# Optimization experiments

Hardware: AMD Instinct MI355X
Metric: run time of the kernel (lower is better)

The kernel has to match this reference:

```python
import jax, jax.numpy as jnp
import numpy as np

D_MODEL, N_HEADS, HEAD_DIM = 384, 12, 32
N_QP, N_VP = 4, 8
B, L = 2, 1024
OUT_DIM = N_HEADS * (HEAD_DIM + N_VP * 3 + N_VP)  # 12*(32+24+8)=768
LN_EPS = 1e-5


def _linear_params(key, din, dout):
    kw, _ = jax.random.split(key)
    W = jax.random.normal(kw, (din, dout), dtype=jnp.float32) / np.sqrt(din).astype(np.float32)
    b = jnp.zeros((dout,), dtype=jnp.float32)
    return W, b


def setup_inputs() -> dict:
    key = jax.random.key(0)
    ks = jax.random.split(key, 12)
    s = jax.random.normal(ks[0], (B, L, D_MODEL), dtype=jnp.float32)
    translations = jax.random.normal(ks[1], (B, L, 3), dtype=jnp.float32)
    # proper rotation-ish matrices via QR of random gaussians
    g = jax.random.normal(ks[2], (B, L, 3, 3), dtype=jnp.float32)
    rotations, _ = jnp.linalg.qr(g)
    mask = jnp.ones((B, L), dtype=bool)
    Wq, bq = _linear_params(ks[3], D_MODEL, N_HEADS * HEAD_DIM)
    Wk, bk = _linear_params(ks[4], D_MODEL, N_HEADS * HEAD_DIM)
    Wv, bv = _linear_params(ks[5], D_MODEL, N_HEADS * HEAD_DIM)
    Wqp, bqp = _linear_params(ks[6], D_MODEL, N_HEADS * N_QP * 3)
    Wkp, bkp = _linear_params(ks[7], D_MODEL, N_HEADS * N_QP * 3)
    Wvp, bvp = _linear_params(ks[8], D_MODEL, N_HEADS * N_VP * 3)
    Wo, bo = _linear_params(ks[9], OUT_DIM, D_MODEL)
    head_weights = jnp.zeros((N_HEADS,), dtype=jnp.float32)
    ln_g = jnp.ones((D_MODEL,), dtype=jnp.float32)
    ln_b = jnp.zeros((D_MODEL,), dtype=jnp.float32)
    return dict(s=s, translations=translations, rotations=rotations, mask=mask,
                ln_g=ln_g, ln_b=ln_b, Wq=Wq, bq=bq, Wk=Wk, bk=bk, Wv=Wv, bv=bv,
                Wqp=Wqp, bqp=bqp, Wkp=Wkp, bkp=bkp, Wvp=Wvp, bvp=bvp,
                head_weights=head_weights, Wo=Wo, bo=bo)


def _ipa(s, translations, rotations, mask, ln_g, ln_b, Wq, bq, Wk, bk, Wv, bv,
         Wqp, bqp, Wkp, bkp, Wvp, bvp, head_weights, Wo, bo):
    Bc, Lc, _ = s.shape
    # LayerNorm
    mu = jnp.mean(s, axis=-1, keepdims=True)
    var = jnp.mean((s - mu) ** 2, axis=-1, keepdims=True)
    h = (s - mu) * jax.lax.rsqrt(var + LN_EPS) * ln_g + ln_b

    q_s = (h @ Wq + bq).reshape(Bc, Lc, N_HEADS, HEAD_DIM)
    k_s = (h @ Wk + bk).reshape(Bc, Lc, N_HEADS, HEAD_DIM)
    v_s = (h @ Wv + bv).reshape(Bc, Lc, N_HEADS, HEAD_DIM)
    q_pts = (h @ Wqp + bqp).reshape(Bc, Lc, N_HEADS, N_QP, 3)
    k_pts = (h @ Wkp + bkp).reshape(Bc, Lc, N_HEADS, N_QP, 3)
    v_pts = (h @ Wvp + bvp).reshape(Bc, Lc, N_HEADS, N_VP, 3)

    T = translations[:, :, None, None, :]  # (B,L,1,1,3)
    # local -> global: out_d = sum_c p_c R_{cd}  (matches torch einsum 'blhpc,blhpcd')
    q_g = jnp.einsum('blhpc,blcd->blhpd', q_pts, rotations) + T
    k_g = jnp.einsum('blhpc,blcd->blhpd', k_pts, rotations) + T
    v_g = jnp.einsum('blhpc,blcd->blhpd', v_pts, rotations) + T

    scalar_attn = jnp.einsum('bihd,bjhd->bhij', q_s, k_s) / np.sqrt(HEAD_DIM).astype(np.float32)

    # sum_{p,c} (q_i - k_j)^2 = |q_i|^2 + |k_j|^2 - 2 q_i.k_j  (avoids B,H,L,L,P,3 tensor)
    q2 = jnp.einsum('bihpc,bihpc->bhi', q_g, q_g)
    k2 = jnp.einsum('bjhpc,bjhpc->bhj', k_g, k_g)
    cross = jnp.einsum('bihpc,bjhpc->bhij', q_g, k_g)
    pt_dists = q2[:, :, :, None] + k2[:, :, None, :] - 2.0 * cross  # (B,H,L,L)

    w_h = jax.nn.softplus(head_weights)[None, :, None, None]
    attn_logits = scalar_attn - 0.5 * w_h * pt_dists
    attn_logits = jnp.where(mask[:, None, None, :], attn_logits, -jnp.inf)
    attn = jax.nn.softmax(attn_logits, axis=-1)  # (B,H,L,L)

    result_scalar = jnp.einsum('bhij,bjhd->bihd', attn, v_s).reshape(Bc, Lc, N_HEADS * HEAD_DIM)
    result_pts = jnp.einsum('bhij,bjhpc->bihpc', attn, v_g)  # (B,L,H,VP,3)
    # global -> local with R^T: out_d = sum_c x_c (R^T)_{cd} = sum_c x_c R_{dc}
    result_pts_local = jnp.einsum('blhpc,bldc->blhpd', result_pts - T, rotations)
    result_pts_norm = jnp.sqrt(jnp.sum(result_pts_local ** 2, axis=-1))  # (B,L,H,VP)

    output = jnp.concatenate([
        result_scalar,
        result_pts_local.reshape(Bc, Lc, N_HEADS * N_VP * 3),
        result_pts_norm.reshape(Bc, Lc, N_HEADS * N_VP),
    ], axis=-1)
    return s + output @ Wo + bo


def reference(s, translations, rotations, mask, ln_g, ln_b, Wq, bq, Wk, bk, Wv, bv,
              Wqp, bqp, Wkp, bkp, Wvp, bvp, head_weights, Wo, bo):
    return _ipa(s, translations, rotations, mask, ln_g, ln_b, Wq, bq, Wk, bk, Wv, bv,
                Wqp, bqp, Wkp, bkp, Wvp, bvp, head_weights, Wo, bo)
```

## Files before the change

### kernel.cpp

```cpp
#include <hip/hip_runtime.h>
#include <hip/hip_bf16.h>

constexpr int B_ = 2, L_ = 1024, D_ = 384, H_ = 12, HD_ = 32;
constexpr int NQP = 4, NVP = 8;
constexpr int ROWS = B_ * L_;
constexpr int PROJ_N = 1728;
constexpr int OUTD = 768;
constexpr int KAUG = 48;
constexpr int C_QS = 0, C_KS = 384, C_VS = 768, C_QP = 1152, C_KP = 1296, C_VP = 1440;

constexpr size_t OFF_HH   = 0;
constexpr size_t OFF_HL   = OFF_HH   + (size_t)ROWS * D_ / 2;
constexpr size_t OFF_WTH  = OFF_HL   + (size_t)ROWS * D_ / 2;
constexpr size_t OFF_WTL  = OFF_WTH  + (size_t)PROJ_N * D_ / 2;
constexpr size_t OFF_BC   = OFF_WTL  + (size_t)PROJ_N * D_ / 2;
constexpr size_t OFF_P    = OFF_BC   + PROJ_N;
constexpr size_t OFF_QPK  = OFF_P    + (size_t)ROWS * PROJ_N;
constexpr size_t QP_FL    = (size_t)24 * 1024 * KAUG / 2;
constexpr size_t OFF_QPL  = OFF_QPK  + QP_FL;
constexpr size_t OFF_KPK  = OFF_QPL  + QP_FL;
constexpr size_t OFF_KPL2 = OFF_KPK  + QP_FL;
constexpr size_t OFF_VT   = OFF_KPL2 + (size_t)24 * 1024 * 16 / 2;
constexpr size_t OFF_OH   = OFF_VT   + (size_t)24 * 64 * L_ / 2;
constexpr size_t OFF_WOH  = OFF_OH   + (size_t)ROWS * OUTD / 2;

typedef __attribute__((ext_vector_type(8)))  __bf16        bf16x8;
typedef __attribute__((ext_vector_type(16))) float         f32x16;
typedef __attribute__((ext_vector_type(4)))  unsigned int  u32x4;
typedef __attribute__((ext_vector_type(8)))  unsigned short us8;

__device__ __forceinline__ unsigned short f2bf(float x) {
    unsigned u = __builtin_bit_cast(unsigned, x);
    unsigned r = (u + 0x7FFFu + ((u >> 16) & 1u)) >> 16;
    return (unsigned short)r;
}
__device__ __forceinline__ float bf2f(unsigned short s) {
    return __builtin_bit_cast(float, (unsigned)s << 16);
}

#define MFMA(a, b, c) __builtin_amdgcn_mfma_f32_32x32x16_bf16((a), (b), (c), 0, 0, 0)
#define CVTPK(dst, x, y) asm("v_cvt_pk_bf16_f32 %0, %1, %2" : "=v"(dst) : "v"(x), "v"(y))
#define PSWAP(a, b) asm("v_permlane32_swap_b32 %0, %1" : "+v"(a), "+v"(b))

typedef const __attribute__((address_space(1))) void* gas_cp;
typedef __attribute__((address_space(3))) void* las_p;
__device__ __forceinline__ void gload16(const void* g, void* l) {
    __builtin_amdgcn_global_load_lds((gas_cp)g, (las_p)l, 16, 0, 0);
}

__global__ __launch_bounds__(256) void setup_kernel(
    const float* __restrict__ s, const float* __restrict__ g,
    const float* __restrict__ bln,
    const float* __restrict__ Wq, const float* __restrict__ Wk, const float* __restrict__ Wv,
    const float* __restrict__ Wqp, const float* __restrict__ Wkp, const float* __restrict__ Wvp,
    const float* __restrict__ bq, const float* __restrict__ bk, const float* __restrict__ bv,
    const float* __restrict__ bqp, const float* __restrict__ bkp, const float* __restrict__ bvp,
    const float* __restrict__ Wo,
    unsigned short* __restrict__ Hhi, unsigned short* __restrict__ Hlo,
    unsigned short* __restrict__ Wthi, unsigned short* __restrict__ Wtlo,
    float* __restrict__ bcat, unsigned short* __restrict__ Wothi)
{
    __shared__ float T[64][65];
    const int blk = blockIdx.x;
    const int tid = threadIdx.x;

    if (blk < 512) {
        const int wave = tid >> 6, lane = tid & 63;
        const int row = blk * 4 + wave;
        const float* sr = s + (size_t)row * D_;
        float v[6];
        float sum = 0.f, sumsq = 0.f;
#pragma unroll
        for (int e = 0; e < 6; ++e) {
            v[e] = sr[lane + e * 64];
            sum += v[e]; sumsq += v[e] * v[e];
        }
#pragma unroll
        for (int o = 32; o >= 1; o >>= 1) {
            sum   += __shfl_xor(sum, o, 64);
            sumsq += __shfl_xor(sumsq, o, 64);
        }
        const float mu  = sum * (1.f / D_);
        const float var = sumsq * (1.f / D_) - mu * mu;
        const float rstd = rsqrtf(var + 1e-5f);
#pragma unroll
        for (int e = 0; e < 6; ++e) {
            const int d = lane + e * 64;
            const float hv = (v[e] - mu) * rstd * g[d] + bln[d];
            const unsigned short h16 = f2bf(hv);
            Hhi[(size_t)row * D_ + d] = h16;
            Hlo[(size_t)row * D_ + d] = f2bf(hv - bf2f(h16));
        }
        return;
    }

    if (blk < 674) {
        const int q = blk - 512;
        const int n0 = (q % 27) * 64, k0 = (q / 27) * 64;
        const int nn = tid & 63, kk4 = tid >> 6;
#pragma unroll
        for (int p = 0; p < 16; ++p) {
            const int k = k0 + p * 4 + kk4, n = n0 + nn;
            float v;
            if      (n < 384)  v = Wq [k * 384 + n];
            else if (n < 768)  v = Wk [k * 384 + n - 384];
            else if (n < 1152) v = Wv [k * 384 + n - 768];
            else if (n < 1296) v = Wqp[k * 144 + n - 1152];
            else if (n < 1440) v = Wkp[k * 144 + n - 1296];
            else               v = Wvp[k * 288 + n - 1440];
            T[p * 4 + kk4][nn] = v;
        }
        if (k0 == 0 && tid < 64) {
            const int n = n0 + tid;
            float v;
            if      (n < 384)  v = bq [n];
            else if (n < 768)  v = bk [n - 384];
            else if (n < 1152) v = bv [n - 768];
            else if (n < 1296) v = bqp[n - 1152];
            else if (n < 1440) v = bkp[n - 1296];
            else               v = bvp[n - 1440];
            bcat[n] = v;
        }
        __syncthreads();
        const int nr = tid >> 2, c = tid & 3;
#pragma unroll
        for (int e = 0; e < 2; ++e) {
            const int kc = e * 4 + c;
            us8 hi8, lo8;
#pragma unroll
            for (int x = 0; x < 8; ++x) {
                const float v = T[kc * 8 + x][nr];
                const unsigned short h16 = f2bf(v);
                hi8[x] = h16; lo8[x] = f2bf(v - bf2f(h16));
            }
            const size_t off = (size_t)(n0 + nr) * D_ + k0 + kc * 8;
            *reinterpret_cast<us8*>(Wthi + off) = hi8;
            *reinterpret_cast<us8*>(Wtlo + off) = lo8;
        }
        return;
    }

    {
        const int q = blk - 674;
        const int n0 = (q % 6) * 64, k0 = (q / 6) * 64;
        const int nn = tid & 63, kk4 = tid >> 6;
#pragma unroll
        for (int p = 0; p < 16; ++p) {
            const int k = k0 + p * 4 + kk4;
            T[p * 4 + kk4][nn] = Wo[(size_t)k * D_ + n0 + nn];
        }
        __syncthreads();
        const int nr = tid >> 2, c = tid & 3;
#pragma unroll
        for (int e = 0; e < 2; ++e) {
            const int kc = e * 4 + c;
            us8 hi8;
#pragma unroll
            for (int x = 0; x < 8; ++x) hi8[x] = f2bf(T[kc * 8 + x][nr]);
            *reinterpret_cast<us8*>(Wothi + (size_t)(n0 + nr) * OUTD + k0 + kc * 8) = hi8;
        }
    }
}

template<int BK, int CMODE>
__global__ __launch_bounds__(256) void lgemm_kernel(
    const unsigned short* __restrict__ Ahi, const unsigned short* __restrict__ Alo,
    const unsigned short* __restrict__ Bhi, const unsigned short* __restrict__ Blo,
    const float* __restrict__ bias, const float* __restrict__ resid,
    float* __restrict__ C, int M, int N, int K)
{
    constexpr int NTILES = (CMODE == 0) ? 2 : 4;
    constexpr int CPR = BK / 8;
    constexpr int RM = CPR - 1;
    constexpr int TILE_US = 64 * BK;
    constexpr int ISS = (TILE_US / 8) / 256;
    __shared__ unsigned short lds[3 * NTILES * TILE_US];

    const int nb = N / 64;
    int wg = blockIdx.x;
    wg = (wg & 7) * ((int)gridDim.x >> 3) + (wg >> 3);
    const int by = wg / nb, bx = wg - by * nb;
    const bool comp = (CMODE == 2 && bx >= 18 && bx <= 22);
    const int m0 = by * 64, n0 = bx * 64;
    const int tid = threadIdx.x;
    const int lane = tid & 63, wv = tid >> 6;
    const int lo31 = lane & 31, hi2 = lane >> 5;
    const int wm = wv >> 1, wn = wv & 1;

    const unsigned short* gsrc[4] = {Ahi, Bhi, Alo ? Alo : Ahi, Blo ? Blo : Bhi};
    const int tb0[4] = {m0, n0, m0, n0};

    auto STAGE = [&](int buf, int t) {
#pragma unroll
        for (int tt = 0; tt < NTILES; ++tt) {
            if (tt >= 2 && !comp) continue;
#pragma unroll
            for (int i = 0; i < ISS; ++i) {
                const int q = i * 256 + tid;
                const int row = q / CPR, c = q & RM;
                const unsigned short* gp = gsrc[tt] +
                    (size_t)(tb0[tt] + row) * K + t * BK + ((c ^ (row & RM)) * 8);
                gload16(gp, &lds[(size_t)(buf * NTILES + tt) * TILE_US + (size_t)q * 8]);
            }
        }
    };

    f32x16 acc;
#pragma unroll
    for (int r = 0; r < 16; ++r) acc[r] = 0.f;

    const int arow = wm * 32 + lo31, brow = wn * 32 + lo31;
    auto COMPUTE = [&](int buf) {
        const char* base = (const char*)&lds[(size_t)buf * NTILES * TILE_US];
#pragma unroll
        for (int ks = 0; ks < BK / 16; ++ks) {
            const int cc = ks * 2 + hi2;
            const int aoff = arow * (BK * 2) + ((cc ^ (arow & RM)) * 16);
            const int boff = brow * (BK * 2) + ((cc ^ (brow & RM)) * 16);
            const bf16x8 ah = *reinterpret_cast<const bf16x8*>(base + aoff);
            const bf16x8 bh = *reinterpret_cast<const bf16x8*>(base + TILE_US * 2 + boff);
            acc = MFMA(ah, bh, acc);
            if (NTILES == 4 && comp) {
                const bf16x8 al = *reinterpret_cast<const bf16x8*>(base + 2 * TILE_US * 2 + aoff);
                const bf16x8 bl = *reinterpret_cast<const bf16x8*>(base + 3 * TILE_US * 2 + boff);
                acc = MFMA(ah, bl, acc);
                acc = MFMA(al, bh, acc);
            }
        }
    };

    constexpr int LPS_P = 2 * ISS;
    constexpr int LPS_C = 4 * ISS;
    auto WAIT_LPS = [&]() {
        if (!comp) {
            if constexpr (LPS_P == 2)
                asm volatile("s_waitcnt vmcnt(2) lgkmcnt(0)" ::: "memory");
            else
                asm volatile("s_waitcnt vmcnt(4) lgkmcnt(0)" ::: "memory");
        } else {
            if constexpr (LPS_C == 4)
                asm volatile("s_waitcnt vmcnt(4) lgkmcnt(0)" ::: "memory");
            else
                asm volatile("s_waitcnt vmcnt(8) lgkmcnt(0)" ::: "memory");
        }
    };

    const int NK = K / BK;
    STAGE(0, 0);
    STAGE(1, 1);
    WAIT_LPS();
    __builtin_amdgcn_s_barrier();
#pragma unroll 1
    for (int t = 0; t < NK; ++t) {
        if (t + 2 < NK) STAGE((t + 2) % 3, t + 2);
        COMPUTE(t % 3);
        if (t + 2 < NK) WAIT_LPS();
        else asm volatile("s_waitcnt vmcnt(0) lgkmcnt(0)" ::: "memory");
        __builtin_amdgcn_s_barrier();
    }

    const int col = n0 + wn * 32 + lo31;
    const float bb = bias ? bias[col] : 0.f;
#pragma unroll
    for (int r = 0; r < 16; ++r) {
        const int row = m0 + wm * 32 + (r & 3) + 8 * (r >> 2) + 4 * hi2;
        float v = acc[r] + bb;
        if (resid) v += resid[(size_t)row * N + col];
        C[(size_t)row * N + col] = v;
    }
}

__global__ __launch_bounds__(64) void prep_kernel(
    const float* __restrict__ P, const float* __restrict__ trans,
    const float* __restrict__ rot, const float* __restrict__ hw,
    unsigned short* __restrict__ Qpk, unsigned short* __restrict__ Qpl,
    unsigned short* __restrict__ Kpk, unsigned short* __restrict__ Kpl2,
    unsigned short* __restrict__ Vt)
{
    __shared__ unsigned short VL[56 * 72];
    const int lane = threadIdx.x;
    const int bh = blockIdx.x >> 4, jc = blockIdx.x & 15;
    const int h = bh % H_, b = bh / H_;
    const int j = jc * 64 + lane;
    const int row = b * L_ + j;

    float R[9], T[3];
#pragma unroll
    for (int u = 0; u < 9; ++u) R[u] = rot[(size_t)row * 9 + u];
#pragma unroll
    for (int u = 0; u < 3; ++u) T[u] = trans[(size_t)row * 3 + u];
    const float* prow = P + (size_t)row * PROJ_N;

    const float w  = log1pf(expf(hw[h]));
    const float mw = -0.5f * w;
    const float qsc = 0.17677669529663687f;

    float Aq[KAUG], Bk[KAUG];
#pragma unroll
    for (int d = 0; d < KAUG; ++d) { Aq[d] = 0.f; Bk[d] = 0.f; }
    const float4* qs4 = reinterpret_cast<const float4*>(prow + C_QS + h * 32);
    const float4* ks4 = reinterpret_cast<const float4*>(prow + C_KS + h * 32);
#pragma unroll
    for (int i = 0; i < 8; ++i) {
        const float4 q = qs4[i], k = ks4[i];
        Aq[i * 4 + 0] = q.x * qsc; Aq[i * 4 + 1] = q.y * qsc;
        Aq[i * 4 + 2] = q.z * qsc; Aq[i * 4 + 3] = q.w * qsc;
        Bk[i * 4 + 0] = k.x; Bk[i * 4 + 1] = k.y;
        Bk[i * 4 + 2] = k.z; Bk[i * 4 + 3] = k.w;
    }
    float qp[12], kp[12];
#pragma unroll
    for (int i = 0; i < 3; ++i) {
        const float4 q = reinterpret_cast<const float4*>(prow + C_QP + h * 12)[i];
        const float4 k = reinterpret_cast<const float4*>(prow + C_KP + h * 12)[i];
        qp[i * 4 + 0] = q.x; qp[i * 4 + 1] = q.y; qp[i * 4 + 2] = q.z; qp[i * 4 + 3] = q.w;
        kp[i * 4 + 0] = k.x; kp[i * 4 + 1] = k.y; kp[i * 4 + 2] = k.z; kp[i * 4 + 3] = k.w;
    }
    float k2 = 0.f;
#pragma unroll
    for (int p = 0; p < NQP; ++p) {
        const float qx = qp[p * 3], qy = qp[p * 3 + 1], qz = qp[p * 3 + 2];
        const float kx = kp[p * 3], ky = kp[p * 3 + 1], kz = kp[p * 3 + 2];
#pragma unroll
        for (int c = 0; c < 3; ++c) {
            const float gq = fmaf(qx, R[0 + c], fmaf(qy, R[3 + c], fmaf(qz, R[6 + c], T[c])));
            const float gk = fmaf(kx, R[0 + c], fmaf(ky, R[3 + c], fmaf(kz, R[6 + c], T[c])));
            Aq[32 + p * 3 + c] = w * gq;
            Bk[32 + p * 3 + c] = gk;
            k2 += gk * gk;
        }
    }
    Aq[44] = mw;
    Bk[44] = k2;

    const size_t ro = ((size_t)bh * L_ + j) * KAUG;
#pragma unroll
    for (int g8 = 0; g8 < 6; ++g8) {
        us8 qh, kh;
#pragma unroll
        for (int e = 0; e < 8; ++e) {
            qh[e] = f2bf(Aq[g8 * 8 + e]);
            kh[e] = f2bf(Bk[g8 * 8 + e]);
        }
        *reinterpret_cast<us8*>(Qpk + ro + g8 * 8) = qh;
        *reinterpret_cast<us8*>(Kpk + ro + g8 * 8) = kh;
        if (g8 >= 4) {
            us8 ql;
#pragma unroll
            for (int e = 0; e < 8; ++e) {
                const float aq = Aq[g8 * 8 + e];
                ql[e] = f2bf(aq - bf2f(f2bf(aq)));
            }
            *reinterpret_cast<us8*>(Qpl + ro + g8 * 8) = ql;
        }
    }
    const size_t ro2 = ((size_t)bh * L_ + j) * 16;
#pragma unroll
    for (int g8 = 0; g8 < 2; ++g8) {
        us8 kl;
#pragma unroll
        for (int e = 0; e < 8; ++e) {
            const float bk = Bk[32 + g8 * 8 + e];
            kl[e] = f2bf(bk - bf2f(f2bf(bk)));
        }
        *reinterpret_cast<us8*>(Kpl2 + ro2 + g8 * 8) = kl;
    }

    const float4* vs4 = reinterpret_cast<const float4*>(prow + C_VS + h * 32);
#pragma unroll
    for (int i = 0; i < 8; ++i) {
        const float4 v = vs4[i];
        VL[(i * 4 + 0) * 72 + lane] = f2bf(v.x);
        VL[(i * 4 + 1) * 72 + lane] = f2bf(v.y);
        VL[(i * 4 + 2) * 72 + lane] = f2bf(v.z);
        VL[(i * 4 + 3) * 72 + lane] = f2bf(v.w);
    }
    float vpt[24];
#pragma unroll
    for (int i = 0; i < 6; ++i) {
        const float4 v = reinterpret_cast<const float4*>(prow + C_VP + h * 24)[i];
        vpt[i * 4 + 0] = v.x; vpt[i * 4 + 1] = v.y; vpt[i * 4 + 2] = v.z; vpt[i * 4 + 3] = v.w;
    }
#pragma unroll
    for (int p = 0; p < NVP; ++p) {
        const float x = vpt[p * 3], y = vpt[p * 3 + 1], z = vpt[p * 3 + 2];
#pragma unroll
        for (int c = 0; c < 3; ++c) {
            const float g = fmaf(x, R[0 + c], fmaf(y, R[3 + c], fmaf(z, R[6 + c], T[c])));
            VL[(32 + p * 3 + c) * 72 + lane] = f2bf(g);
        }
    }
    __syncthreads();
#pragma unroll
    for (int e = 0; e < 8; ++e) {
        const int ch = lane + 64 * e;
        const int vd = ch >> 3, jj = (ch & 7) * 8;
        us8 val;
        if (vd < 56) {
            val = *reinterpret_cast<const us8*>(&VL[vd * 72 + jj]);
        } else {
            for (int x = 0; x < 8; ++x) val[x] = 0;
        }
        *reinterpret_cast<us8*>(Vt + (size_t)(bh * 64 + vd) * L_ + jc * 64 + jj) = val;
    }
}

struct KV { bf16x8 kh0, kh1, kh2, kl2, v00, v01, v10, v11; };

#define LOADT(F, t) do {                                                      \
    const char* _kp = khp + (size_t)(t) * 3072;                               \
    (F).kh0 = *reinterpret_cast<const bf16x8*>(_kp);                          \
    (F).kh1 = *reinterpret_cast<const bf16x8*>(_kp + 32);                     \
    (F).kh2 = *reinterpret_cast<const bf16x8*>(_kp + 64);                     \
    (F).kl2 = *reinterpret_cast<const bf16x8*>(klp + (size_t)(t) * 1024);     \
    const char* _vp = vp + (size_t)(t) * 64;                                  \
    (F).v00 = *reinterpret_cast<const bf16x8*>(_vp);                          \
    (F).v01 = *reinterpret_cast<const bf16x8*>(_vp + 32);                     \
    (F).v10 = *reinterpret_cast<const bf16x8*>(_vp + 65536);                  \
    (F).v11 = *reinterpret_cast<const bf16x8*>(_vp + 65536 + 32);             \
} while (0)

__device__ __forceinline__ void proc_tile(
    const KV& F, const bf16x8& q0h, const bf16x8& q1h, const bf16x8& q2h,
    const bf16x8& q2l, f32x16& o0, f32x16& o1, float& m, float& lsum)
{
    f32x16 d;
#pragma unroll
    for (int r = 0; r < 16; ++r) d[r] = 0.f;
    d = MFMA(F.kh0, q0h, d);
    d = MFMA(F.kh1, q1h, d);
    d = MFMA(F.kh2, q2h, d); d = MFMA(F.kh2, q2l, d);
    d = MFMA(F.kl2, q2h, d);

    float pmax = d[0];
#pragma unroll
    for (int r = 1; r < 16; ++r) pmax = fmaxf(pmax, d[r]);
    pmax = fmaxf(pmax, __shfl_xor(pmax, 32));
    const float mn = fmaxf(m, pmax);
    const float scale = __expf(m - mn);
    float p[16];
    float ps = 0.f;
#pragma unroll
    for (int r = 0; r < 16; ++r) { p[r] = __expf(d[r] - mn); ps += p[r]; }
    lsum = fmaf(lsum, scale, ps);
    m = mn;
#pragma unroll
    for (int r = 0; r < 16; ++r) { o0[r] *= scale; o1[r] *= scale; }

    unsigned W0, W1, W2, W3, X0, X1, X2, X3;
    CVTPK(W0, p[0], p[1]);  CVTPK(W1, p[2], p[3]);
    CVTPK(W2, p[4], p[5]);  CVTPK(W3, p[6], p[7]);
    PSWAP(W0, W2);          PSWAP(W1, W3);
    CVTPK(X0, p[8], p[9]);  CVTPK(X1, p[10], p[11]);
    CVTPK(X2, p[12], p[13]); CVTPK(X3, p[14], p[15]);
    PSWAP(X0, X2);          PSWAP(X1, X3);
    const u32x4 u0 = {W0, W1, W2, W3};
    const u32x4 u1 = {X0, X1, X2, X3};
    const bf16x8 pb0 = __builtin_bit_cast(bf16x8, u0);
    const bf16x8 pb1 = __builtin_bit_cast(bf16x8, u1);

    o0 = MFMA(F.v00, pb0, o0);
    o1 = MFMA(F.v10, pb0, o1);
    o0 = MFMA(F.v01, pb1, o0);
    o1 = MFMA(F.v11, pb1, o1);
}

__global__ __launch_bounds__(256) void attn_kernel(
    const unsigned short* __restrict__ Qpk, const unsigned short* __restrict__ Qpl,
    const unsigned short* __restrict__ Kpk, const unsigned short* __restrict__ Kpl2,
    const unsigned short* __restrict__ Vt,
    const float* __restrict__ trans, const float* __restrict__ rot,
    unsigned short* __restrict__ Ophi)
{
    __shared__ float MRG[4 * 64 * 36];
    const int wg = ((int)blockIdx.x & 7) * 96 + ((int)blockIdx.x >> 3);
    const int bh = wg >> 5, itile = wg & 31;
    const int h = bh % H_, b = bh / H_;
    const int tid = threadIdx.x;
    const int wv = tid >> 6, lane = tid & 63;
    const int lo31 = lane & 31, hi = lane >> 5;

    const char* qkp = (const char*)Qpk + ((size_t)(bh * L_ + itile * 32 + lo31) * KAUG + hi * 8) * 2;
    const char* qlp = (const char*)Qpl + ((size_t)(bh * L_ + itile * 32 + lo31) * KAUG + hi * 8) * 2;
    const bf16x8 q0h = *reinterpret_cast<const bf16x8*>(qkp);
    const bf16x8 q1h = *reinterpret_cast<const bf16x8*>(qkp + 32);
    const bf16x8 q2h = *reinterpret_cast<const bf16x8*>(qkp + 64);
    const bf16x8 q2l = *reinterpret_cast<const bf16x8*>(qlp + 64);

    const char* khp = (const char*)Kpk  + ((size_t)(bh * L_ + lo31) * KAUG + hi * 8) * 2;
    const char* klp = (const char*)Kpl2 + ((size_t)(bh * L_ + lo31) * 16 + hi * 8) * 2;
    const char* vp  = (const char*)Vt   + ((size_t)bh * 64 * L_ + (size_t)lo31 * L_ + hi * 8) * 2;

    f32x16 o0, o1;
#pragma unroll
    for (int r = 0; r < 16; ++r) { o0[r] = 0.f; o1[r] = 0.f; }
    float m = -3.0e38f, lsum = 0.f;

    const int t0 = wv * 8;
    KV fa, fb;
    LOADT(fa, t0);
#pragma unroll 1
    for (int tt = 0; tt < 8; tt += 2) {
        LOADT(fb, t0 + tt + 1);
        proc_tile(fa, q0h, q1h, q2h, q2l, o0, o1, m, lsum);
        if (tt + 2 < 8) LOADT(fa, t0 + tt + 2);
        proc_tile(fb, q0h, q1h, q2h, q2l, o0, o1, m, lsum);
    }

    if (wv != 0) {
        const int base = (wv * 64 + lane) * 36;
#pragma unroll
        for (int r = 0; r < 16; ++r) {
            MRG[base + r] = o0[r];
            MRG[base + 16 + r] = o1[r];
        }
        MRG[base + 32] = m;
        MRG[base + 33] = lsum;
    }
    __syncthreads();
    if (wv != 0) return;

#pragma unroll
    for (int w = 1; w < 4; ++w) {
        const int b2 = (w * 64 + lane) * 36;
        const float mw_ = MRG[b2 + 32], lw = MRG[b2 + 33];
        const float nm = fmaxf(m, mw_);
        const float s0 = __expf(m - nm), s1 = __expf(mw_ - nm);
#pragma unroll
        for (int r = 0; r < 16; ++r) {
            o0[r] = o0[r] * s0 + MRG[b2 + r] * s1;
            o1[r] = o1[r] * s0 + MRG[b2 + 16 + r] * s1;
        }
        lsum = lsum * s0 + lw * s1;
        m = nm;
    }

    lsum += __shfl_xor(lsum, 32);
    const float inv = 1.f / lsum;
    const int row = b * L_ + itile * 32 + lo31;
    unsigned short* ophr = Ophi + (size_t)row * OUTD + h * HD_;
#pragma unroll
    for (int r = 0; r < 16; ++r) {
        const int vd = (r & 3) + 8 * (r >> 2) + 4 * hi;
        ophr[vd] = f2bf(o0[r] * inv);
    }

    float own[12], oth[12];
#pragma unroll
    for (int r = 0; r < 12; ++r) {
        own[r] = o1[r] * inv;
        oth[r] = __shfl_xor(own[r], 32);
    }
    float dims[24];
#pragma unroll
    for (int vd = 0; vd < 24; ++vd) {
        const int r = (vd & 3) + 4 * (vd >> 3);
        const int hb = (vd >> 2) & 1;
        dims[vd] = (hi == hb) ? own[r] : oth[r];
    }
    float R[9], T[3];
#pragma unroll
    for (int u = 0; u < 9; ++u) R[u] = rot[(size_t)row * 9 + u];
#pragma unroll
    for (int u = 0; u < 3; ++u) T[u] = trans[(size_t)row * 3 + u];
    unsigned short* orow = Ophi + (size_t)row * OUTD;
    auto finpt = [&](float x, float y, float z, int hp) {
        x -= T[0]; y -= T[1]; z -= T[2];
        const float lx = fmaf(x, R[0], fmaf(y, R[1], z * R[2]));
        const float ly = fmaf(x, R[3], fmaf(y, R[4], z * R[5]));
        const float lz = fmaf(x, R[6], fmaf(y, R[7], z * R[8]));
        orow[384 + hp * 3 + 0] = f2bf(lx);
        orow[384 + hp * 3 + 1] = f2bf(ly);
        orow[384 + hp * 3 + 2] = f2bf(lz);
        orow[672 + hp] = f2bf(sqrtf(lx * lx + ly * ly + lz * lz));
    };
    if (hi == 0) {
        finpt(dims[0],  dims[1],  dims[2],  h * 8 + 0);
        finpt(dims[3],  dims[4],  dims[5],  h * 8 + 1);
        finpt(dims[6],  dims[7],  dims[8],  h * 8 + 2);
        finpt(dims[9],  dims[10], dims[11], h * 8 + 3);
    } else {
        finpt(dims[12], dims[13], dims[14], h * 8 + 4);
        finpt(dims[15], dims[16], dims[17], h * 8 + 5);
        finpt(dims[18], dims[19], dims[20], h * 8 + 6);
        finpt(dims[21], dims[22], dims[23], h * 8 + 7);
    }
}

extern "C" void kernel_launch(void* const* d_in, const int* in_sizes, int n_in,
                              void* d_out, int out_size, void* d_ws, size_t ws_size,
                              hipStream_t stream)
{
    const float* s     = (const float*)d_in[0];
    const float* trans = (const float*)d_in[1];
    const float* rot   = (const float*)d_in[2];
    const float* ln_g  = (const float*)d_in[4];
    const float* ln_b  = (const float*)d_in[5];
    const float* Wq  = (const float*)d_in[6];  const float* bq  = (const float*)d_in[7];
    const float* Wk  = (const float*)d_in[8];  const float* bk  = (const float*)d_in[9];
    const float* Wv  = (const float*)d_in[10]; const float* bv  = (const float*)d_in[11];
    const float* Wqp = (const float*)d_in[12]; const float* bqp = (const float*)d_in[13];
    const float* Wkp = (const float*)d_in[14]; const float* bkp = (const float*)d_in[15];
    const float* Wvp = (const float*)d_in[16]; const float* bvp = (const float*)d_in[17];
    const float* hw  = (const float*)d_in[18];
    const float* Wo  = (const float*)d_in[19]; const float* bo  = (const float*)d_in[20];
    (void)in_sizes; (void)n_in; (void)out_size; (void)ws_size;

    float* ws = (float*)d_ws;
    unsigned short* Hhi   = (unsigned short*)(ws + OFF_HH);
    unsigned short* Hlo   = (unsigned short*)(ws + OFF_HL);
    unsigned short* Wthi  = (unsigned short*)(ws + OFF_WTH);
    unsigned short* Wtlo  = (unsigned short*)(ws + OFF_WTL);
    float* bc  = ws + OFF_BC;
    float* P   = ws + OFF_P;
    unsigned short* Qpk   = (unsigned short*)(ws + OFF_QPK);
    unsigned short* Qpl   = (unsigned short*)(ws + OFF_QPL);
    unsigned short* Kpk   = (unsigned short*)(ws + OFF_KPK);
    unsigned short* Kpl2  = (unsigned short*)(ws + OFF_KPL2);
    unsigned short* Vt    = (unsigned short*)(ws + OFF_VT);
    unsigned short* Ophi  = (unsigned short*)(ws + OFF_OH);
    unsigned short* Wothi = (unsigned short*)(ws + OFF_WOH);
    float* out = (float*)d_out;

    setup_kernel<<<746, 256, 0, stream>>>(
        s, ln_g, ln_b, Wq, Wk, Wv, Wqp, Wkp, Wvp,
        bq, bk, bv, bqp, bkp, bvp, Wo,
        Hhi, Hlo, Wthi, Wtlo, bc, Wothi);
    lgemm_kernel<32, 2><<<(ROWS / 64) * (PROJ_N / 64), 256, 0, stream>>>(
        Hhi, Hlo, Wthi, Wtlo, bc, nullptr, P, ROWS, PROJ_N, D_);
    prep_kernel<<<24 * 16, 64, 0, stream>>>(
        P, trans, rot, hw, Qpk, Qpl, Kpk, Kpl2, Vt);
    attn_kernel<<<B_ * H_ * (L_ / 32), 256, 0, stream>>>(
        Qpk, Qpl, Kpk, Kpl2, Vt, trans, rot, Ophi);
    lgemm_kernel<64, 0><<<(ROWS / 64) * (D_ / 64), 256, 0, stream>>>(
        Ophi, nullptr, Wothi, nullptr, bo, s, out, ROWS, D_, OUTD);
}
```

Before: 72.79 us.

## Reorder projection GEMM tiles and use small-tile single-wave output GEMM

The projection GEMM now remaps workgroup indices so that the heavier compensated (hi/lo) tiles in columns 18-22 are scheduled first, with the plain tiles after them, to balance load. The output projection GEMM is replaced by a new one-wavefront kernel using 32x32 tiles, giving 768 small workgroups instead of 192 to raise parallelism on the many CUs. The new kernel has no barrier between stages, relying on each wave waiting only on its own loads. WAIT_LPS is also simplified to fixed vmcnt values.

```diff
diff --git a/kernel.cpp b/kernel.cpp
--- a/kernel.cpp
+++ b/kernel.cpp
@@ -179,7 +179,12 @@
     const int nb = N / 64;
     int wg = blockIdx.x;
     wg = (wg & 7) * ((int)gridDim.x >> 3) + (wg >> 3);
-    const int by = wg / nb, bx = wg - by * nb;
+    int by, bx;
+    if (CMODE == 2) {
+        if (wg < 160) { by = wg / 5; bx = 18 + wg % 5; }
+        else { const int u = wg - 160; by = u / 22; const int t2 = u % 22;
+               bx = (t2 < 18) ? t2 : t2 + 5; }
+    } else { by = wg / nb; bx = wg - by * nb; }
     const bool comp = (CMODE == 2 && bx >= 18 && bx <= 22);
     const int m0 = by * 64, n0 = bx * 64;
     const int tid = threadIdx.x;
@@ -229,20 +234,9 @@
         }
     };
 
-    constexpr int LPS_P = 2 * ISS;
-    constexpr int LPS_C = 4 * ISS;
     auto WAIT_LPS = [&]() {
-        if (!comp) {
-            if constexpr (LPS_P == 2)
-                asm volatile("s_waitcnt vmcnt(2) lgkmcnt(0)" ::: "memory");
-            else
-                asm volatile("s_waitcnt vmcnt(4) lgkmcnt(0)" ::: "memory");
-        } else {
-            if constexpr (LPS_C == 4)
-                asm volatile("s_waitcnt vmcnt(4) lgkmcnt(0)" ::: "memory");
-            else
-                asm volatile("s_waitcnt vmcnt(8) lgkmcnt(0)" ::: "memory");
-        }
+        if (!comp) asm volatile("s_waitcnt vmcnt(2) lgkmcnt(0)" ::: "memory");
+        else       asm volatile("s_waitcnt vmcnt(4) lgkmcnt(0)" ::: "memory");
     };
 
     const int NK = K / BK;
@@ -267,6 +261,78 @@
         float v = acc[r] + bb;
         if (resid) v += resid[(size_t)row * N + col];
         C[(size_t)row * N + col] = v;
+    }
+}
+
+__global__ __launch_bounds__(64, 4) void sgemm_kernel(
+    const unsigned short* __restrict__ Ahi, const unsigned short* __restrict__ Bhi,
+    const float* __restrict__ bias, const float* __restrict__ resid,
+    float* __restrict__ C, int M, int N, int K)
+{
+    constexpr int BK = 64;
+    constexpr int RM = BK / 8 - 1;
+    constexpr int TILE_US = 32 * BK;
+    __shared__ unsigned short lds[3 * 2 * TILE_US];
+
+    const int nb = N / 32;
+    int wg = blockIdx.x;
+    wg = (wg & 7) * ((int)gridDim.x >> 3) + (wg >> 3);
+    const int by = wg / nb, bx = wg - by * nb;
+    const int m0 = by * 32, n0 = bx * 32;
+    const int lane = threadIdx.x;
+    const int lo31 = lane & 31, hi2 = lane >> 5;
+
+    auto STAGE = [&](int buf, int t) {
+#pragma unroll
+        for (int i = 0; i < 4; ++i) {
+            const int q = i * 64 + lane;
+            const int row = q >> 3, c = q & 7;
+            gload16(Ahi + (size_t)(m0 + row) * K + t * BK + ((c ^ (row & RM)) * 8),
+                    &lds[(size_t)(buf * 2) * TILE_US + (size_t)q * 8]);
+        }
+#pragma unroll
+        for (int i = 0; i < 4; ++i) {
+            const int q = i * 64 + lane;
+            const int row = q >> 3, c = q & 7;
+            gload16(Bhi + (size_t)(n0 + row) * K + t * BK + ((c ^ (row & RM)) * 8),
+                    &lds[(size_t)(buf * 2 + 1) * TILE_US + (size_t)q * 8]);
+        }
+    };
+
+    f32x16 acc;
+#pragma unroll
+    for (int r = 0; r < 16; ++r) acc[r] = 0.f;
+
+    auto COMPUTE = [&](int buf) {
+        const char* base = (const char*)&lds[(size_t)buf * 2 * TILE_US];
+#pragma unroll
+        for (int ks = 0; ks < BK / 16; ++ks) {
+            const int cc = ks * 2 + hi2;
+            const int off = lo31 * (BK * 2) + ((cc ^ (lo31 & RM)) * 16);
+            const bf16x8 ah = *reinterpret_cast<const bf16x8*>(base + off);
+            const bf16x8 bh = *reinterpret_cast<const bf16x8*>(base + TILE_US * 2 + off);
+            acc = MFMA(ah, bh, acc);
+        }
+    };
+
+    const int NK = K / BK;
+    STAGE(0, 0);
+    STAGE(1, 1);
+    asm volatile("s_waitcnt vmcnt(8)" ::: "memory");
+#pragma unroll 1
+    for (int t = 0; t < NK; ++t) {
+        if (t + 2 < NK) STAGE((t + 2) % 3, t + 2);
+        COMPUTE(t % 3);
+        if (t + 2 < NK) asm volatile("s_waitcnt vmcnt(8)" ::: "memory");
+        else            asm volatile("s_waitcnt vmcnt(0)" ::: "memory");
+    }
+
+    const int col = n0 + lo31;
+    const float bb = bias[col];
+#pragma unroll
+    for (int r = 0; r < 16; ++r) {
+        const int row = m0 + (r & 3) + 8 * (r >> 2) + 4 * hi2;
+        C[(size_t)row * N + col] = acc[r] + bb + resid[(size_t)row * N + col];
     }
 }
 
@@ -632,6 +698,6 @@
         P, trans, rot, hw, Qpk, Qpl, Kpk, Kpl2, Vt);
     attn_kernel<<<B_ * H_ * (L_ / 32), 256, 0, stream>>>(
         Qpk, Qpl, Kpk, Kpl2, Vt, trans, rot, Ophi);
-    lgemm_kernel<64, 0><<<(ROWS / 64) * (D_ / 64), 256, 0, stream>>>(
-        Ophi, nullptr, Wothi, nullptr, bo, s, out, ROWS, D_, OUTD);
-}
+    sgemm_kernel<<<(ROWS / 32) * (D_ / 32), 64, 0, stream>>>(
+        Ophi, Wothi, bo, s, out, ROWS, D_, OUTD);
+}
```

Result: no change. 72.55 us (-0.3%).
